# Kernel optimization log

Hardware: AMD Instinct MI355X
Metric: run time of the kernel (lower is better)

The kernel has to match this reference:

```python
import jax, jax.numpy as jnp
import numpy as np

N_HEADS = 16
HEAD_DIM = 64
D_MODEL = N_HEADS * HEAD_DIM
MASK_NUM = -2.0**32 + 1.0
LN_EPS = 1e-8


def setup_inputs() -> dict:
    key = jax.random.key(0)
    ks = jax.random.split(key, 6)
    B, S = 2, 2048
    queries = jax.random.normal(ks[0], (B, S, D_MODEL), dtype=jnp.float32)
    keys = jax.random.normal(ks[1], (B, S, D_MODEL), dtype=jnp.float32)
    values = jax.random.normal(ks[2], (B, S, D_MODEL), dtype=jnp.float32)
    lim = np.sqrt(6.0 / (D_MODEL + D_MODEL)).astype(np.float32)  # glorot_uniform
    Wq = jax.random.uniform(ks[3], (D_MODEL, D_MODEL), jnp.float32, -lim, lim)
    Wk = jax.random.uniform(ks[4], (D_MODEL, D_MODEL), jnp.float32, -lim, lim)
    Wv = jax.random.uniform(ks[5], (D_MODEL, D_MODEL), jnp.float32, -lim, lim)
    gamma = jnp.ones((D_MODEL,), jnp.float32)
    beta = jnp.zeros((D_MODEL,), jnp.float32)
    return {"queries": queries, "keys": keys, "values": values,
            "Wq": Wq, "Wk": Wk, "Wv": Wv, "gamma": gamma, "beta": beta}


def _split_heads(x):
    # [B, S, H*dh] -> tf.split(axis=2)+concat(axis=0) order: [H*B, S, dh]
    B, S, _ = x.shape
    return x.reshape(B, S, N_HEADS, HEAD_DIM).transpose(2, 0, 1, 3).reshape(N_HEADS * B, S, HEAD_DIM)


def _merge_heads(x, B):
    # [H*B, S, dh] -> [B, S, H*dh]
    S = x.shape[1]
    return x.reshape(N_HEADS, B, S, HEAD_DIM).transpose(1, 2, 0, 3).reshape(B, S, D_MODEL)


def reference(queries, keys, values, Wq, Wk, Wv, gamma, beta):
    B = queries.shape[0]
    q = _split_heads(queries @ Wq)   # [HB, Sq, dh]
    k = _split_heads(keys @ Wk)      # [HB, Sk, dh]
    v = _split_heads(values @ Wv)    # [HB, Sk, dh]

    scores = jnp.einsum('bqd,bkd->bqk', q, k) / jnp.float32(np.sqrt(HEAD_DIM))
    # key padding mask: positions whose projected key is all-zero
    kmask = jnp.sign(jnp.sum(jnp.abs(k), axis=-1))  # [HB, Sk]
    scores = jnp.where(kmask[:, None, :] == 0, jnp.float32(MASK_NUM), scores)
    attn = jax.nn.softmax(scores, axis=-1)
    # query mask: zero out rows whose projected query is all-zero
    qmask = jnp.sign(jnp.sum(jnp.abs(q), axis=-1))  # [HB, Sq]
    attn = attn * qmask[:, :, None]
    att_out = jnp.einsum('bqk,bkd->bqd', attn, v)   # [HB, Sq, dh]
    att_out = _merge_heads(att_out, B)               # [B, Sq, D]

    x = att_out + queries
    mean = jnp.mean(x, axis=-1, keepdims=True)
    var = jnp.mean((x - mean) ** 2, axis=-1, keepdims=True)
    norm = (x - mean) / jnp.sqrt(var + LN_EPS)
    return gamma * norm + beta
```

## Files before the change

kernel.cpp:

```cpp
#include <hip/hip_runtime.h>

#define DM   1024
#define SEQ  2048
#define NH   16
#define HD   64
#define ROWS 4096

typedef unsigned short u16;
typedef unsigned int   u32;
typedef __attribute__((ext_vector_type(8))) __bf16 bf16x8;
typedef __attribute__((ext_vector_type(4))) float  f32x4;
typedef __attribute__((ext_vector_type(16))) float f32x16;

__device__ __forceinline__ u16 f2bf(float f) {
  u32 u = __builtin_bit_cast(u32, f);
  u += 0x7fffu + ((u >> 16) & 1u);
  return (u16)(u >> 16);
}

__device__ __forceinline__ void async16(const void* g, void* lds) {
  __builtin_amdgcn_global_load_lds((const __attribute__((address_space(1))) u32*)g,
                                   (__attribute__((address_space(3))) u32*)lds, 16, 0, 0);
}


__global__ __launch_bounds__(256) void k_cvt_act(const float* __restrict__ q,
                                                 const float* __restrict__ k,
                                                 const float* __restrict__ v,
                                                 u16* __restrict__ dst) {
  const float* src = blockIdx.z == 0 ? q : (blockIdx.z == 1 ? k : v);
  u16* d = dst + (size_t)blockIdx.z * ((size_t)ROWS * DM);
  size_t i = ((size_t)blockIdx.x * 256 + threadIdx.x) * 8;
  float4 a = *(const float4*)(src + i);
  float4 b = *(const float4*)(src + i + 4);
  u32 w0 = (u32)f2bf(a.x) | ((u32)f2bf(a.y) << 16);
  u32 w1 = (u32)f2bf(a.z) | ((u32)f2bf(a.w) << 16);
  u32 w2 = (u32)f2bf(b.x) | ((u32)f2bf(b.y) << 16);
  u32 w3 = (u32)f2bf(b.z) | ((u32)f2bf(b.w) << 16);
  uint4 o4; o4.x = w0; o4.y = w1; o4.z = w2; o4.w = w3;
  *(uint4*)(d + i) = o4;
}

__global__ __launch_bounds__(256) void k_cvt_wt(const float* __restrict__ Wq,
                                                const float* __restrict__ Wk,
                                                const float* __restrict__ Wv,
                                                u16* __restrict__ wt) {
  __shared__ float t[32][33];
  const float* W = blockIdx.z == 0 ? Wq : (blockIdx.z == 1 ? Wk : Wv);
  u16* D = wt + (size_t)blockIdx.z * (DM * DM);
  int bx = blockIdx.x * 32, by = blockIdx.y * 32;
  int x = threadIdx.x, y = threadIdx.y;
  for (int i = 0; i < 32; i += 8) t[y + i][x] = W[(size_t)(by + y + i) * DM + bx + x];
  __syncthreads();
  for (int i = 0; i < 32; i += 8) D[(size_t)(bx + y + i) * DM + by + x] = f2bf(t[x][y + i]);
}


__global__ __launch_bounds__(256) void k_gemm(const u16* __restrict__ Abase,
                                              const u16* __restrict__ Btbase,
                                              u16* __restrict__ Cbase) {
  __shared__ u16 As[128 * 32];
  __shared__ u16 Bs[128 * 32];
  const int z = blockIdx.z;
  const u16* A  = Abase  + (size_t)z * ((size_t)ROWS * DM);
  const u16* Bt = Btbase + (size_t)z * (DM * DM);
  u16* C        = Cbase  + (size_t)z * ((size_t)ROWS * DM);
  const float sc = (z == 0) ? 0.18033688011112043f : 1.0f;
  int tid = threadIdx.x, w = tid >> 6, l = tid & 63;
  int fr = l & 15, fq = l >> 4;
  int bid = blockIdx.y * 8 + blockIdx.x;
  int nb  = (bid & 7) * 32 + (bid >> 3);
  int m0 = (nb >> 3) * 128, n0 = (nb & 7) * 128;
  int wr = (w >> 1) * 64, wc = (w & 1) * 64;
  f32x4 acc[4][4];
  for (int i = 0; i < 4; ++i) for (int j = 0; j < 4; ++j) acc[i][j] = (f32x4){0.f, 0.f, 0.f, 0.f};

  for (int k0 = 0; k0 < DM; k0 += 32) {
    __syncthreads();
    for (int c = 0; c < 2; ++c) {
      int loff = (c * 4 + w) * 1024;
      int eoff = (loff >> 1) + l * 8;
      int row = eoff >> 5;
      int blk = (eoff & 31) >> 3;
      int gblk = blk ^ ((row >> 1) & 3);
      async16(A  + (size_t)(m0 + row) * DM + k0 + (gblk << 3), (char*)As + loff);
      async16(Bt + (size_t)(n0 + row) * DM + k0 + (gblk << 3), (char*)Bs + loff);
    }
    __syncthreads();
    bf16x8 af[4], bf[4];
    for (int i = 0; i < 4; ++i) {
      int row = wr + i * 16 + fr;
      af[i] = *(const bf16x8*)(As + row * 32 + ((fq ^ ((row >> 1) & 3)) << 3));
    }
    for (int j = 0; j < 4; ++j) {
      int row = wc + j * 16 + fr;
      bf[j] = *(const bf16x8*)(Bs + row * 32 + ((fq ^ ((row >> 1) & 3)) << 3));
    }
    for (int i = 0; i < 4; ++i)
      for (int j = 0; j < 4; ++j)
        acc[i][j] = __builtin_amdgcn_mfma_f32_16x16x32_bf16(af[i], bf[j], acc[i][j], 0, 0, 0);
  }
  for (int i = 0; i < 4; ++i)
    for (int j = 0; j < 4; ++j)
      for (int jj = 0; jj < 4; ++jj) {
        int row = m0 + wr + i * 16 + fq * 4 + jj;
        int col = n0 + wc + j * 16 + fr;
        C[(size_t)row * DM + col] = f2bf(acc[i][j][jj] * sc);
      }
}


__global__ __launch_bounds__(256) void k_vt(const u16* __restrict__ vproj,
                                            u16* __restrict__ vt) {
  __shared__ u16 t[64][64];
  int y = blockIdx.y;
  int h = y >> 1, b = y & 1;
  int s0 = blockIdx.x * 64;
  int tid = threadIdx.x;
  for (int c = 0; c < 2; ++c) {
    int rr = c * 32 + (tid >> 3);
    int blk = tid & 7;
    uint4 vv = *(const uint4*)(vproj + (size_t)(b * SEQ + s0 + rr) * DM + h * 64 + blk * 8);
    *(uint4*)(&t[rr][((blk ^ (rr & 7)) * 8)]) = vv;
  }
  __syncthreads();
  for (int c = 0; c < 2; ++c) {
    int d = c * 32 + (tid >> 3);
    int p = tid & 7;
    int B = p ^ (d & 7);
    int g = B >> 1, half = B & 1;
    u16 tmp[8];
    for (int j = 0; j < 8; ++j) {
      int kj = (j < 4) ? (4 * half + j) : (8 + 4 * half + (j - 4));
      int ss = 16 * g + kj;
      tmp[j] = t[ss][((d >> 3) ^ (ss & 7)) * 8 + (d & 7)];
    }
    *(uint4*)(vt + (size_t)(y * 64 + d) * SEQ + s0 + p * 8) = *(uint4*)tmp;
  }
}


__global__ __launch_bounds__(256, 4) void k_attn(const u16* __restrict__ Qp,
                                                 const u16* __restrict__ Kp,
                                                 const u16* __restrict__ Vt,
                                                 float* __restrict__ att) {
  __shared__ u16 lds[2][8192];
  const int tid = threadIdx.x, w = tid >> 6, l = tid & 63;
  const int lrow = l & 31, h = l >> 5;
  const int qh = w & 1, kh = w >> 1;
  const int g = blockIdx.x;
  const int vy = (g & 7) * 4 + ((g >> 3) & 3);
  const int vx = g >> 5;
  const int head = vy >> 1, b = vy & 1;
  const int hcol = head * 64;
  const int q0w = vx * 64 + qh * 32;

  const u16* qrow = Qp + (size_t)(b * SEQ + q0w + lrow) * DM + hcol + h * 8;
  bf16x8 qb0 = *(const bf16x8*)(qrow);
  bf16x8 qb1 = *(const bf16x8*)(qrow + 16);
  bf16x8 qb2 = *(const bf16x8*)(qrow + 32);
  bf16x8 qb3 = *(const bf16x8*)(qrow + 48);

  const int sw = lrow & 7;
  const int kbase = kh * 4096 + lrow * 128;
  const int B0 = kbase + (((0 + h) ^ sw) << 4);
  const int B1 = kbase + (((2 + h) ^ sw) << 4);
  const int B2 = kbase + (((4 + h) ^ sw) << 4);
  const int B3 = kbase + (((6 + h) ^ sw) << 4);

  const int vb = 8192 + lrow * 128;
  const int V0 = vb + (((4 * kh + 0 + h) ^ sw) << 4);
  const int V1 = vb + (((4 * kh + 2 + h) ^ sw) << 4);

  const int ldo0 = w * 1024, ldo1 = (4 + w) * 1024;
  const int e0 = (ldo0 >> 1) + l * 8, e1 = (ldo1 >> 1) + l * 8;
  const int r0 = e0 >> 6, r1 = e1 >> 6;
  const int kb0 = ((e0 & 63) >> 3) ^ (r0 & 7), kb1 = ((e1 & 63) >> 3) ^ (r1 & 7);
  const size_t koff0 = (size_t)(b * SEQ + r0) * DM + hcol + kb0 * 8;
  const size_t koff1 = (size_t)(b * SEQ + r1) * DM + hcol + kb1 * 8;
  const size_t voff0 = (size_t)(vy * 64 + r0) * SEQ + (e0 & 63);
  const size_t voff1 = (size_t)(vy * 64 + r1) * SEQ + (e1 & 63);

  const f32x16 kzero = {};
  u32 one2 = 0x3F803F80u;
  uint4 ou; ou.x = one2; ou.y = one2; ou.z = one2; ou.w = one2;
  const bf16x8 onesA = __builtin_bit_cast(bf16x8, ou);

  f32x16 ot0 = {}, ot1 = {}, ssacc = {};

  {
    char* dst = (char*)(&lds[0][0]);
    async16(Kp + koff0, dst + ldo0);
    async16(Kp + koff1, dst + ldo1);
    async16(Vt + voff0, dst + 8192 + ldo0);
    async16(Vt + voff1, dst + 8192 + ldo1);
  }
  __syncthreads();

  int cur = 0;
  for (int t = 0; t < SEQ / 64; ++t) {
    if (t != SEQ / 64 - 1) {
      char* dst = (char*)(&lds[cur ^ 1][0]);
      size_t kadv = (size_t)(t + 1) * (64 * DM);
      size_t vadv = (size_t)(t + 1) * 64;
      async16(Kp + kadv + koff0, dst + ldo0);
      async16(Kp + kadv + koff1, dst + ldo1);
      async16(Vt + vadv + voff0, dst + 8192 + ldo0);
      async16(Vt + vadv + voff1, dst + 8192 + ldo1);
    }

    const char* Kb = (const char*)(&lds[cur][0]);
    bf16x8 a0 = *(const bf16x8*)(Kb + B0);
    bf16x8 a1 = *(const bf16x8*)(Kb + B1);
    bf16x8 a2 = *(const bf16x8*)(Kb + B2);
    bf16x8 a3 = *(const bf16x8*)(Kb + B3);
    __builtin_amdgcn_s_setprio(1);
    f32x16 st = __builtin_amdgcn_mfma_f32_32x32x16_bf16(a0, qb0, kzero, 0, 0, 0);
    st = __builtin_amdgcn_mfma_f32_32x32x16_bf16(a1, qb1, st, 0, 0, 0);
    st = __builtin_amdgcn_mfma_f32_32x32x16_bf16(a2, qb2, st, 0, 0, 0);
    st = __builtin_amdgcn_mfma_f32_32x32x16_bf16(a3, qb3, st, 0, 0, 0);
    __builtin_amdgcn_s_setprio(0);

    f32x16 p;
#pragma unroll
    for (int i = 0; i < 16; ++i) p[i] = __builtin_amdgcn_exp2f(st[i]);

    bf16x8 pb0, pb1;
#pragma unroll
    for (int j = 0; j < 8; ++j) {
      pb0[j] = (__bf16)p[j];
      pb1[j] = (__bf16)p[8 + j];
    }

    bf16x8 vf0 = *(const bf16x8*)(Kb + V0);
    bf16x8 vf1 = *(const bf16x8*)(Kb + V1);
    bf16x8 vf2 = *(const bf16x8*)(Kb + 4096 + V0);
    bf16x8 vf3 = *(const bf16x8*)(Kb + 4096 + V1);
    __builtin_amdgcn_s_setprio(1);
    ot0 = __builtin_amdgcn_mfma_f32_32x32x16_bf16(vf0, pb0, ot0, 0, 0, 0);
    ot0 = __builtin_amdgcn_mfma_f32_32x32x16_bf16(vf1, pb1, ot0, 0, 0, 0);
    ot1 = __builtin_amdgcn_mfma_f32_32x32x16_bf16(vf2, pb0, ot1, 0, 0, 0);
    ot1 = __builtin_amdgcn_mfma_f32_32x32x16_bf16(vf3, pb1, ot1, 0, 0, 0);
    ssacc = __builtin_amdgcn_mfma_f32_32x32x16_bf16(onesA, pb0, ssacc, 0, 0, 0);
    ssacc = __builtin_amdgcn_mfma_f32_32x32x16_bf16(onesA, pb1, ssacc, 0, 0, 0);
    __builtin_amdgcn_s_setprio(0);

    __syncthreads();
    cur ^= 1;
  }

  const float lacc = ssacc[0];

  float* mrg = (float*)&lds[0][0];
  const int slot = qh * 2176;
  if (kh) {
#pragma unroll
    for (int r = 0; r < 16; ++r) {
      mrg[slot + r * 64 + l] = ot0[r];
      mrg[slot + (16 + r) * 64 + l] = ot1[r];
    }
    mrg[slot + 2048 + l] = lacc;
  }
  __syncthreads();
  if (!kh) {
    float inv = 1.f / (lacc + mrg[slot + 2048 + l]);
    float* orow = att + (size_t)(b * SEQ + q0w + lrow) * DM + hcol + 4 * h;
#pragma unroll
    for (int G = 0; G < 4; ++G) {
      float4 w0;
      w0.x = (ot0[4 * G + 0] + mrg[slot + (4 * G + 0) * 64 + l]) * inv;
      w0.y = (ot0[4 * G + 1] + mrg[slot + (4 * G + 1) * 64 + l]) * inv;
      w0.z = (ot0[4 * G + 2] + mrg[slot + (4 * G + 2) * 64 + l]) * inv;
      w0.w = (ot0[4 * G + 3] + mrg[slot + (4 * G + 3) * 64 + l]) * inv;
      *(float4*)(orow + 8 * G) = w0;
      float4 w1;
      w1.x = (ot1[4 * G + 0] + mrg[slot + (16 + 4 * G + 0) * 64 + l]) * inv;
      w1.y = (ot1[4 * G + 1] + mrg[slot + (16 + 4 * G + 1) * 64 + l]) * inv;
      w1.z = (ot1[4 * G + 2] + mrg[slot + (16 + 4 * G + 2) * 64 + l]) * inv;
      w1.w = (ot1[4 * G + 3] + mrg[slot + (16 + 4 * G + 3) * 64 + l]) * inv;
      *(float4*)(orow + 32 + 8 * G) = w1;
    }
  }
}


__global__ __launch_bounds__(256) void k_ln(const float* __restrict__ att,
                                            const float* __restrict__ qin,
                                            const float* __restrict__ gamma,
                                            const float* __restrict__ beta,
                                            float* __restrict__ out) {
  __shared__ float rsum[4], rsum2[4];
  int row = blockIdx.x, t = threadIdx.x;
  size_t off = (size_t)row * DM + t * 4;
  float4 a = *(const float4*)(att + off);
  float4 q = *(const float4*)(qin + off);
  float4 x; x.x = a.x + q.x; x.y = a.y + q.y; x.z = a.z + q.z; x.w = a.w + q.w;
  float s = x.x + x.y + x.z + x.w;
  float s2 = x.x * x.x + x.y * x.y + x.z * x.z + x.w * x.w;
  for (int o2 = 1; o2 < 64; o2 <<= 1) { s += __shfl_xor(s, o2); s2 += __shfl_xor(s2, o2); }
  int w = t >> 6, l = t & 63;
  if (l == 0) { rsum[w] = s; rsum2[w] = s2; }
  __syncthreads();
  s = rsum[0] + rsum[1] + rsum[2] + rsum[3];
  s2 = rsum2[0] + rsum2[1] + rsum2[2] + rsum2[3];
  float mean = s * (1.f / DM);
  float var = s2 * (1.f / DM) - mean * mean;
  float rstd = rsqrtf(var + 1e-8f);
  float4 g = *(const float4*)(gamma + t * 4);
  float4 be = *(const float4*)(beta + t * 4);
  float4 r;
  r.x = (x.x - mean) * rstd * g.x + be.x;
  r.y = (x.y - mean) * rstd * g.y + be.y;
  r.z = (x.z - mean) * rstd * g.z + be.z;
  r.w = (x.w - mean) * rstd * g.w + be.w;
  *(float4*)(out + off) = r;
}


extern "C" void kernel_launch(void* const* d_in, const int* in_sizes, int n_in,
                              void* d_out, int out_size, void* d_ws, size_t ws_size,
                              hipStream_t stream) {
  (void)in_sizes; (void)n_in; (void)out_size; (void)ws_size;
  const float* q     = (const float*)d_in[0];
  const float* k     = (const float*)d_in[1];
  const float* v     = (const float*)d_in[2];
  const float* Wq    = (const float*)d_in[3];
  const float* Wk    = (const float*)d_in[4];
  const float* Wv    = (const float*)d_in[5];
  const float* gamma = (const float*)d_in[6];
  const float* beta  = (const float*)d_in[7];
  float* out = (float*)d_out;
  char* ws = (char*)d_ws;

  const size_t ACT_B = 3ull * ROWS * DM * 2;
  const size_t WT_B  = 3ull * DM * DM * 2;

  u16* actb  = (u16*)ws;
  u16* wtb   = (u16*)(ws + ACT_B);
  u16* projb = (u16*)(ws + ACT_B + WT_B);
  u16* vt    = (u16*)ws;
  float* att = (float*)(ws + 8ull * 1024 * 1024);

  k_cvt_act<<<dim3(2048, 1, 3), 256, 0, stream>>>(q, k, v, actb);
  k_cvt_wt<<<dim3(32, 32, 3), dim3(32, 8), 0, stream>>>(Wq, Wk, Wv, wtb);
  k_gemm<<<dim3(8, 32, 3), 256, 0, stream>>>(actb, wtb, projb);
  k_vt<<<dim3(SEQ / 64, NH * 2), 256, 0, stream>>>(projb + 2ull * ROWS * DM, vt);
  k_attn<<<1024, 256, 0, stream>>>(projb, projb + (size_t)ROWS * DM, vt, att);
  k_ln<<<ROWS, 256, 0, stream>>>(att, q, gamma, beta, out);
}
```

Before: 116.7 us.

## Software-pipeline PV MFMA behind next QK, deepen GEMM K-tile, drop ones-MFMA rowsum

The attention loop now issues the previous tile's P·V MFMAs after the current tile's QK MFMAs, so exp2 and bf16 conversion can overlap matrix work. To support this, V uses a triple-buffered LDS ring. The row sum is now accumulated with VALU adds plus one cross-half shuffle, replacing two extra MFMAs against a ones matrix, and offsets are narrowed to 32-bit. Separately, the projection GEMM's K tile grows from 32 to 64 with an 8-way XOR swizzle, which halves barrier count per K but doubles LDS use.

Measured after the change: 119.7 us. +2.5%, slower.

```diff
diff --git a/kernel.cpp b/kernel.cpp
--- a/kernel.cpp
+++ b/kernel.cpp
@@ -59,8 +59,8 @@
 __global__ __launch_bounds__(256) void k_gemm(const u16* __restrict__ Abase,
                                               const u16* __restrict__ Btbase,
                                               u16* __restrict__ Cbase) {
-  __shared__ u16 As[128 * 32];
-  __shared__ u16 Bs[128 * 32];
+  __shared__ u16 As[128 * 64];
+  __shared__ u16 Bs[128 * 64];
   const int z = blockIdx.z;
   const u16* A  = Abase  + (size_t)z * ((size_t)ROWS * DM);
   const u16* Bt = Btbase + (size_t)z * (DM * DM);
@@ -75,30 +75,32 @@
   f32x4 acc[4][4];
   for (int i = 0; i < 4; ++i) for (int j = 0; j < 4; ++j) acc[i][j] = (f32x4){0.f, 0.f, 0.f, 0.f};
 
-  for (int k0 = 0; k0 < DM; k0 += 32) {
+  for (int k0 = 0; k0 < DM; k0 += 64) {
     __syncthreads();
-    for (int c = 0; c < 2; ++c) {
+    for (int c = 0; c < 4; ++c) {
       int loff = (c * 4 + w) * 1024;
       int eoff = (loff >> 1) + l * 8;
-      int row = eoff >> 5;
-      int blk = (eoff & 31) >> 3;
-      int gblk = blk ^ ((row >> 1) & 3);
+      int row = eoff >> 6;
+      int blk = (eoff & 63) >> 3;
+      int gblk = blk ^ (row & 7);
       async16(A  + (size_t)(m0 + row) * DM + k0 + (gblk << 3), (char*)As + loff);
       async16(Bt + (size_t)(n0 + row) * DM + k0 + (gblk << 3), (char*)Bs + loff);
     }
     __syncthreads();
-    bf16x8 af[4], bf[4];
-    for (int i = 0; i < 4; ++i) {
-      int row = wr + i * 16 + fr;
-      af[i] = *(const bf16x8*)(As + row * 32 + ((fq ^ ((row >> 1) & 3)) << 3));
-    }
-    for (int j = 0; j < 4; ++j) {
-      int row = wc + j * 16 + fr;
-      bf[j] = *(const bf16x8*)(Bs + row * 32 + ((fq ^ ((row >> 1) & 3)) << 3));
-    }
-    for (int i = 0; i < 4; ++i)
-      for (int j = 0; j < 4; ++j)
-        acc[i][j] = __builtin_amdgcn_mfma_f32_16x16x32_bf16(af[i], bf[j], acc[i][j], 0, 0, 0);
+    for (int ks = 0; ks < 2; ++ks) {
+      bf16x8 af[4], bf[4];
+      for (int i = 0; i < 4; ++i) {
+        int row = wr + i * 16 + fr;
+        af[i] = *(const bf16x8*)(As + row * 64 + (((ks * 4 + fq) ^ (row & 7)) << 3));
+      }
+      for (int j = 0; j < 4; ++j) {
+        int row = wc + j * 16 + fr;
+        bf[j] = *(const bf16x8*)(Bs + row * 64 + (((ks * 4 + fq) ^ (row & 7)) << 3));
+      }
+      for (int i = 0; i < 4; ++i)
+        for (int j = 0; j < 4; ++j)
+          acc[i][j] = __builtin_amdgcn_mfma_f32_16x16x32_bf16(af[i], bf[j], acc[i][j], 0, 0, 0);
+    }
   }
   for (int i = 0; i < 4; ++i)
     for (int j = 0; j < 4; ++j)
@@ -144,7 +146,7 @@
                                                  const u16* __restrict__ Kp,
                                                  const u16* __restrict__ Vt,
                                                  float* __restrict__ att) {
-  __shared__ u16 lds[2][8192];
+  __shared__ u16 lds[20480];
   const int tid = threadIdx.x, w = tid >> 6, l = tid & 63;
   const int lrow = l & 31, h = l >> 5;
   const int qh = w & 1, kh = w >> 1;
@@ -168,48 +170,48 @@
   const int B2 = kbase + (((4 + h) ^ sw) << 4);
   const int B3 = kbase + (((6 + h) ^ sw) << 4);
 
-  const int vb = 8192 + lrow * 128;
-  const int V0 = vb + (((4 * kh + 0 + h) ^ sw) << 4);
-  const int V1 = vb + (((4 * kh + 2 + h) ^ sw) << 4);
+  const int vfb = lrow * 128;
+  const int V0 = vfb + (((4 * kh + 0 + h) ^ sw) << 4);
+  const int V1 = vfb + (((4 * kh + 2 + h) ^ sw) << 4);
 
   const int ldo0 = w * 1024, ldo1 = (4 + w) * 1024;
   const int e0 = (ldo0 >> 1) + l * 8, e1 = (ldo1 >> 1) + l * 8;
   const int r0 = e0 >> 6, r1 = e1 >> 6;
   const int kb0 = ((e0 & 63) >> 3) ^ (r0 & 7), kb1 = ((e1 & 63) >> 3) ^ (r1 & 7);
-  const size_t koff0 = (size_t)(b * SEQ + r0) * DM + hcol + kb0 * 8;
-  const size_t koff1 = (size_t)(b * SEQ + r1) * DM + hcol + kb1 * 8;
-  const size_t voff0 = (size_t)(vy * 64 + r0) * SEQ + (e0 & 63);
-  const size_t voff1 = (size_t)(vy * 64 + r1) * SEQ + (e1 & 63);
+  const u32 koff0 = (u32)((b * SEQ + r0) * DM + hcol + kb0 * 8);
+  const u32 koff1 = (u32)((b * SEQ + r1) * DM + hcol + kb1 * 8);
+  const u32 voff0 = (u32)((vy * 64 + r0) * SEQ + (e0 & 63));
+  const u32 voff1 = (u32)((vy * 64 + r1) * SEQ + (e1 & 63));
 
   const f32x16 kzero = {};
-  u32 one2 = 0x3F803F80u;
-  uint4 ou; ou.x = one2; ou.y = one2; ou.z = one2; ou.w = one2;
-  const bf16x8 onesA = __builtin_bit_cast(bf16x8, ou);
-
-  f32x16 ot0 = {}, ot1 = {}, ssacc = {};
+  f32x16 ot0 = {}, ot1 = {};
+  float lacc = 0.f;
+  bf16x8 pbP0 = {}, pbP1 = {};
 
   {
-    char* dst = (char*)(&lds[0][0]);
-    async16(Kp + koff0, dst + ldo0);
-    async16(Kp + koff1, dst + ldo1);
-    async16(Vt + voff0, dst + 8192 + ldo0);
-    async16(Vt + voff1, dst + 8192 + ldo1);
-  }
-  __syncthreads();
-
-  int cur = 0;
+    char* base = (char*)lds;
+    async16(Kp + koff0, base + ldo0);
+    async16(Kp + koff1, base + ldo1);
+    async16(Vt + voff0, base + 16384 + ldo0);
+    async16(Vt + voff1, base + 16384 + ldo1);
+  }
+  __syncthreads();
+
+  int vprev = 16384, vcur = 0, vnxt = 8192;
   for (int t = 0; t < SEQ / 64; ++t) {
-    if (t != SEQ / 64 - 1) {
-      char* dst = (char*)(&lds[cur ^ 1][0]);
-      size_t kadv = (size_t)(t + 1) * (64 * DM);
-      size_t vadv = (size_t)(t + 1) * 64;
-      async16(Kp + kadv + koff0, dst + ldo0);
-      async16(Kp + kadv + koff1, dst + ldo1);
-      async16(Vt + vadv + voff0, dst + 8192 + ldo0);
-      async16(Vt + vadv + voff1, dst + 8192 + ldo1);
-    }
-
-    const char* Kb = (const char*)(&lds[cur][0]);
+    char* base = (char*)lds;
+    if (t < SEQ / 64 - 1) {
+      u32 kadv = (u32)(t + 1) * (64 * DM);
+      u32 vadv = (u32)(t + 1) * 64;
+      char* kd = base + ((t + 1) & 1) * 8192;
+      char* vd = base + 16384 + vnxt;
+      async16(Kp + kadv + koff0, kd + ldo0);
+      async16(Kp + kadv + koff1, kd + ldo1);
+      async16(Vt + vadv + voff0, vd + ldo0);
+      async16(Vt + vadv + voff1, vd + ldo1);
+    }
+
+    const char* Kb = base + (t & 1) * 8192;
     bf16x8 a0 = *(const bf16x8*)(Kb + B0);
     bf16x8 a1 = *(const bf16x8*)(Kb + B1);
     bf16x8 a2 = *(const bf16x8*)(Kb + B2);
@@ -221,37 +223,52 @@
     st = __builtin_amdgcn_mfma_f32_32x32x16_bf16(a3, qb3, st, 0, 0, 0);
     __builtin_amdgcn_s_setprio(0);
 
+    if (t) {
+      const char* Vb = base + 16384 + vprev;
+      bf16x8 vf0 = *(const bf16x8*)(Vb + V0);
+      bf16x8 vf1 = *(const bf16x8*)(Vb + V1);
+      bf16x8 vf2 = *(const bf16x8*)(Vb + 4096 + V0);
+      bf16x8 vf3 = *(const bf16x8*)(Vb + 4096 + V1);
+      __builtin_amdgcn_s_setprio(1);
+      ot0 = __builtin_amdgcn_mfma_f32_32x32x16_bf16(vf0, pbP0, ot0, 0, 0, 0);
+      ot0 = __builtin_amdgcn_mfma_f32_32x32x16_bf16(vf1, pbP1, ot0, 0, 0, 0);
+      ot1 = __builtin_amdgcn_mfma_f32_32x32x16_bf16(vf2, pbP0, ot1, 0, 0, 0);
+      ot1 = __builtin_amdgcn_mfma_f32_32x32x16_bf16(vf3, pbP1, ot1, 0, 0, 0);
+      __builtin_amdgcn_s_setprio(0);
+    }
+
     f32x16 p;
 #pragma unroll
     for (int i = 0; i < 16; ++i) p[i] = __builtin_amdgcn_exp2f(st[i]);
-
-    bf16x8 pb0, pb1;
+    float s0 = (p[0] + p[1]) + (p[2] + p[3]);
+    float s1 = (p[4] + p[5]) + (p[6] + p[7]);
+    float s2 = (p[8] + p[9]) + (p[10] + p[11]);
+    float s3 = (p[12] + p[13]) + (p[14] + p[15]);
+    lacc += (s0 + s1) + (s2 + s3);
 #pragma unroll
     for (int j = 0; j < 8; ++j) {
-      pb0[j] = (__bf16)p[j];
-      pb1[j] = (__bf16)p[8 + j];
-    }
-
-    bf16x8 vf0 = *(const bf16x8*)(Kb + V0);
-    bf16x8 vf1 = *(const bf16x8*)(Kb + V1);
-    bf16x8 vf2 = *(const bf16x8*)(Kb + 4096 + V0);
-    bf16x8 vf3 = *(const bf16x8*)(Kb + 4096 + V1);
-    __builtin_amdgcn_s_setprio(1);
-    ot0 = __builtin_amdgcn_mfma_f32_32x32x16_bf16(vf0, pb0, ot0, 0, 0, 0);
-    ot0 = __builtin_amdgcn_mfma_f32_32x32x16_bf16(vf1, pb1, ot0, 0, 0, 0);
-    ot1 = __builtin_amdgcn_mfma_f32_32x32x16_bf16(vf2, pb0, ot1, 0, 0, 0);
-    ot1 = __builtin_amdgcn_mfma_f32_32x32x16_bf16(vf3, pb1, ot1, 0, 0, 0);
-    ssacc = __builtin_amdgcn_mfma_f32_32x32x16_bf16(onesA, pb0, ssacc, 0, 0, 0);
-    ssacc = __builtin_amdgcn_mfma_f32_32x32x16_bf16(onesA, pb1, ssacc, 0, 0, 0);
-    __builtin_amdgcn_s_setprio(0);
+      pbP0[j] = (__bf16)p[j];
+      pbP1[j] = (__bf16)p[8 + j];
+    }
 
     __syncthreads();
-    cur ^= 1;
-  }
-
-  const float lacc = ssacc[0];
-
-  float* mrg = (float*)&lds[0][0];
+    int tmp = vprev; vprev = vcur; vcur = vnxt; vnxt = tmp;
+  }
+
+  {
+    const char* Vb = (const char*)lds + 16384 + vprev;
+    bf16x8 vf0 = *(const bf16x8*)(Vb + V0);
+    bf16x8 vf1 = *(const bf16x8*)(Vb + V1);
+    bf16x8 vf2 = *(const bf16x8*)(Vb + 4096 + V0);
+    bf16x8 vf3 = *(const bf16x8*)(Vb + 4096 + V1);
+    ot0 = __builtin_amdgcn_mfma_f32_32x32x16_bf16(vf0, pbP0, ot0, 0, 0, 0);
+    ot0 = __builtin_amdgcn_mfma_f32_32x32x16_bf16(vf1, pbP1, ot0, 0, 0, 0);
+    ot1 = __builtin_amdgcn_mfma_f32_32x32x16_bf16(vf2, pbP0, ot1, 0, 0, 0);
+    ot1 = __builtin_amdgcn_mfma_f32_32x32x16_bf16(vf3, pbP1, ot1, 0, 0, 0);
+  }
+  lacc += __shfl_xor(lacc, 32);
+
+  float* mrg = (float*)lds;
   const int slot = qh * 2176;
   if (kh) {
 #pragma unroll
```

## Give each attention wave a private K/V tile stream and drop block barriers

Applied to the files above, without the earlier changes.

The attention kernel now gives each wave its own LDS region and a contiguous half of the key range, streaming 32-key K and V tiles. K/V fragments are loaded into registers first, and the next tile's async loads are issued before the MFMAs, so the per-iteration __syncthreads and double buffering go away. The softmax denominator is accumulated with VALU adds plus a cross-half shuffle instead of two extra ones-vector MFMAs per step. The V-transpose kernel's output layout and swizzle change to match the new per-wave tile shape. In exchange, each wave fetches its own K/V data, so the two query groups no longer share loads and global/L2 traffic roughly doubles.

Measured after the change: 125.2 us. 7.3% more time.

```diff
diff --git a/kernel.cpp b/kernel.cpp
--- a/kernel.cpp
+++ b/kernel.cpp
@@ -127,15 +127,16 @@
   for (int c = 0; c < 2; ++c) {
     int d = c * 32 + (tid >> 3);
     int p = tid & 7;
-    int B = p ^ (d & 7);
+    int span = p >> 2;
+    int B = p & 3;
     int g = B >> 1, half = B & 1;
     u16 tmp[8];
     for (int j = 0; j < 8; ++j) {
-      int kj = (j < 4) ? (4 * half + j) : (8 + 4 * half + (j - 4));
-      int ss = 16 * g + kj;
+      int kj = (j < 4) ? (16 * g + 4 * half + j) : (16 * g + 8 + 4 * half + (j - 4));
+      int ss = span * 32 + kj;
       tmp[j] = t[ss][((d >> 3) ^ (ss & 7)) * 8 + (d & 7)];
     }
-    *(uint4*)(vt + (size_t)(y * 64 + d) * SEQ + s0 + p * 8) = *(uint4*)tmp;
+    *(uint4*)(vt + (size_t)(y * 64 + d) * SEQ + s0 + span * 32 + B * 8) = *(uint4*)tmp;
   }
 }
 
@@ -144,16 +145,17 @@
                                                  const u16* __restrict__ Kp,
                                                  const u16* __restrict__ Vt,
                                                  float* __restrict__ att) {
-  __shared__ u16 lds[2][8192];
+  __shared__ u16 lds[16384];
   const int tid = threadIdx.x, w = tid >> 6, l = tid & 63;
   const int lrow = l & 31, h = l >> 5;
-  const int qh = w & 1, kh = w >> 1;
+  const int kh = w & 1, qg = w >> 1;
   const int g = blockIdx.x;
   const int vy = (g & 7) * 4 + ((g >> 3) & 3);
   const int vx = g >> 5;
   const int head = vy >> 1, b = vy & 1;
   const int hcol = head * 64;
-  const int q0w = vx * 64 + qh * 32;
+  const int q0w = vx * 64 + qg * 32;
+  const int wb = w * 8192;
 
   const u16* qrow = Qp + (size_t)(b * SEQ + q0w + lrow) * DM + hcol + h * 8;
   bf16x8 qb0 = *(const bf16x8*)(qrow);
@@ -162,58 +164,67 @@
   bf16x8 qb3 = *(const bf16x8*)(qrow + 48);
 
   const int sw = lrow & 7;
-  const int kbase = kh * 4096 + lrow * 128;
-  const int B0 = kbase + (((0 + h) ^ sw) << 4);
-  const int B1 = kbase + (((2 + h) ^ sw) << 4);
-  const int B2 = kbase + (((4 + h) ^ sw) << 4);
-  const int B3 = kbase + (((6 + h) ^ sw) << 4);
-
-  const int vb = 8192 + lrow * 128;
-  const int V0 = vb + (((4 * kh + 0 + h) ^ sw) << 4);
-  const int V1 = vb + (((4 * kh + 2 + h) ^ sw) << 4);
-
-  const int ldo0 = w * 1024, ldo1 = (4 + w) * 1024;
-  const int e0 = (ldo0 >> 1) + l * 8, e1 = (ldo1 >> 1) + l * 8;
-  const int r0 = e0 >> 6, r1 = e1 >> 6;
-  const int kb0 = ((e0 & 63) >> 3) ^ (r0 & 7), kb1 = ((e1 & 63) >> 3) ^ (r1 & 7);
-  const size_t koff0 = (size_t)(b * SEQ + r0) * DM + hcol + kb0 * 8;
-  const size_t koff1 = (size_t)(b * SEQ + r1) * DM + hcol + kb1 * 8;
-  const size_t voff0 = (size_t)(vy * 64 + r0) * SEQ + (e0 & 63);
-  const size_t voff1 = (size_t)(vy * 64 + r1) * SEQ + (e1 & 63);
+  const int kfb = wb + lrow * 128;
+  const int F0 = kfb + (((0 + h) ^ sw) << 4);
+  const int F1 = kfb + (((2 + h) ^ sw) << 4);
+  const int F2 = kfb + (((4 + h) ^ sw) << 4);
+  const int F3 = kfb + (((6 + h) ^ sw) << 4);
+
+  const int vz0 = (lrow ^ (lrow >> 2)) & 3;
+  const int vz1 = ((lrow + 32) ^ ((lrow + 32) >> 2)) & 3;
+  const int vb0 = wb + 4096 + lrow * 64;
+  const int vb1 = wb + 4096 + (32 + lrow) * 64;
+  const int V00 = vb0 + (((0 + h) ^ vz0) << 4);
+  const int V01 = vb0 + (((2 + h) ^ vz0) << 4);
+  const int V10 = vb1 + (((0 + h) ^ vz1) << 4);
+  const int V11 = vb1 + (((2 + h) ^ vz1) << 4);
+
+  u32 koff[4], voff[4];
+#pragma unroll
+  for (int i = 0; i < 4; ++i) {
+    int e = i * 512 + l * 8;
+    int krow = e >> 6;
+    int gblk = ((e & 63) >> 3) ^ (krow & 7);
+    koff[i] = (u32)((b * SEQ + krow) * DM + hcol + gblk * 8);
+    int d = e >> 5;
+    int gkb = (l & 3) ^ ((d ^ (d >> 2)) & 3);
+    voff[i] = (u32)((vy * 64 + d) * SEQ + gkb * 8);
+  }
+  const u32 kv0 = (u32)(kh * 1024);
 
   const f32x16 kzero = {};
-  u32 one2 = 0x3F803F80u;
-  uint4 ou; ou.x = one2; ou.y = one2; ou.z = one2; ou.w = one2;
-  const bf16x8 onesA = __builtin_bit_cast(bf16x8, ou);
-
-  f32x16 ot0 = {}, ot1 = {}, ssacc = {};
-
-  {
-    char* dst = (char*)(&lds[0][0]);
-    async16(Kp + koff0, dst + ldo0);
-    async16(Kp + koff1, dst + ldo1);
-    async16(Vt + voff0, dst + 8192 + ldo0);
-    async16(Vt + voff1, dst + 8192 + ldo1);
-  }
-  __syncthreads();
-
-  int cur = 0;
-  for (int t = 0; t < SEQ / 64; ++t) {
-    if (t != SEQ / 64 - 1) {
-      char* dst = (char*)(&lds[cur ^ 1][0]);
-      size_t kadv = (size_t)(t + 1) * (64 * DM);
-      size_t vadv = (size_t)(t + 1) * 64;
-      async16(Kp + kadv + koff0, dst + ldo0);
-      async16(Kp + kadv + koff1, dst + ldo1);
-      async16(Vt + vadv + voff0, dst + 8192 + ldo0);
-      async16(Vt + vadv + voff1, dst + 8192 + ldo1);
-    }
-
-    const char* Kb = (const char*)(&lds[cur][0]);
-    bf16x8 a0 = *(const bf16x8*)(Kb + B0);
-    bf16x8 a1 = *(const bf16x8*)(Kb + B1);
-    bf16x8 a2 = *(const bf16x8*)(Kb + B2);
-    bf16x8 a3 = *(const bf16x8*)(Kb + B3);
+  f32x16 ot0 = {}, ot1 = {};
+  float lacc = 0.f;
+
+  char* base = (char*)lds;
+#pragma unroll
+  for (int i = 0; i < 4; ++i) {
+    async16(Kp + (kv0 * DM) + koff[i], base + wb + i * 1024);
+    async16(Vt + kv0 + voff[i],        base + wb + 4096 + i * 1024);
+  }
+  asm volatile("s_waitcnt vmcnt(0)" ::: "memory");
+
+  for (int t = 0; t < 32; ++t) {
+    bf16x8 a0 = *(const bf16x8*)(base + F0);
+    bf16x8 a1 = *(const bf16x8*)(base + F1);
+    bf16x8 a2 = *(const bf16x8*)(base + F2);
+    bf16x8 a3 = *(const bf16x8*)(base + F3);
+    bf16x8 vf0 = *(const bf16x8*)(base + V00);
+    bf16x8 vf1 = *(const bf16x8*)(base + V01);
+    bf16x8 vf2 = *(const bf16x8*)(base + V10);
+    bf16x8 vf3 = *(const bf16x8*)(base + V11);
+    asm volatile("s_waitcnt lgkmcnt(0)" ::: "memory");
+    __builtin_amdgcn_sched_barrier(0);
+
+    if (t + 1 < 32) {
+      u32 kv = kv0 + (u32)(t + 1) * 32u;
+#pragma unroll
+      for (int i = 0; i < 4; ++i) {
+        async16(Kp + (kv * DM) + koff[i], base + wb + i * 1024);
+        async16(Vt + kv + voff[i],        base + wb + 4096 + i * 1024);
+      }
+    }
+
     __builtin_amdgcn_s_setprio(1);
     f32x16 st = __builtin_amdgcn_mfma_f32_32x32x16_bf16(a0, qb0, kzero, 0, 0, 0);
     st = __builtin_amdgcn_mfma_f32_32x32x16_bf16(a1, qb1, st, 0, 0, 0);
@@ -224,7 +235,11 @@
     f32x16 p;
 #pragma unroll
     for (int i = 0; i < 16; ++i) p[i] = __builtin_amdgcn_exp2f(st[i]);
-
+    float s0 = (p[0] + p[1]) + (p[2] + p[3]);
+    float s1 = (p[4] + p[5]) + (p[6] + p[7]);
+    float s2 = (p[8] + p[9]) + (p[10] + p[11]);
+    float s3 = (p[12] + p[13]) + (p[14] + p[15]);
+    lacc += (s0 + s1) + (s2 + s3);
     bf16x8 pb0, pb1;
 #pragma unroll
     for (int j = 0; j < 8; ++j) {
@@ -232,27 +247,20 @@
       pb1[j] = (__bf16)p[8 + j];
     }
 
-    bf16x8 vf0 = *(const bf16x8*)(Kb + V0);
-    bf16x8 vf1 = *(const bf16x8*)(Kb + V1);
-    bf16x8 vf2 = *(const bf16x8*)(Kb + 4096 + V0);
-    bf16x8 vf3 = *(const bf16x8*)(Kb + 4096 + V1);
     __builtin_amdgcn_s_setprio(1);
     ot0 = __builtin_amdgcn_mfma_f32_32x32x16_bf16(vf0, pb0, ot0, 0, 0, 0);
     ot0 = __builtin_amdgcn_mfma_f32_32x32x16_bf16(vf1, pb1, ot0, 0, 0, 0);
     ot1 = __builtin_amdgcn_mfma_f32_32x32x16_bf16(vf2, pb0, ot1, 0, 0, 0);
     ot1 = __builtin_amdgcn_mfma_f32_32x32x16_bf16(vf3, pb1, ot1, 0, 0, 0);
-    ssacc = __builtin_amdgcn_mfma_f32_32x32x16_bf16(onesA, pb0, ssacc, 0, 0, 0);
-    ssacc = __builtin_amdgcn_mfma_f32_32x32x16_bf16(onesA, pb1, ssacc, 0, 0, 0);
     __builtin_amdgcn_s_setprio(0);
 
-    __syncthreads();
-    cur ^= 1;
-  }
-
-  const float lacc = ssacc[0];
-
-  float* mrg = (float*)&lds[0][0];
-  const int slot = qh * 2176;
+    asm volatile("s_waitcnt vmcnt(0)" ::: "memory");
+  }
+  lacc += __shfl_xor(lacc, 32);
+
+  __syncthreads();
+  float* mrg = (float*)lds;
+  const int slot = qg * 2176;
   if (kh) {
 #pragma unroll
     for (int r = 0; r < 16; ++r) {
```
